# Kernel optimization log

Measured on AMD Instinct MI355X. Metric: run time of the kernel, lower is better.

The kernel has to match this reference:

```python
import jax, jax.numpy as jnp
import numpy as np

HEADS = 16
DHEAD = 128
B, S, DMODEL = 2, 2048, 2048


def setup_inputs() -> dict:
    key = jax.random.key(0)
    k1, k2, k3 = jax.random.split(key, 3)
    x = jax.random.normal(k1, (B, S, DMODEL), dtype=jnp.float32)
    # Linear weights, stored as [in, out] so forward is x @ w (no bias).
    w_in = jax.random.normal(k2, (DMODEL, 3 * HEADS * DHEAD), dtype=jnp.float32) * (DMODEL ** -0.5)
    w_out = jax.random.normal(k3, (HEADS * DHEAD, DMODEL), dtype=jnp.float32) * ((HEADS * DHEAD) ** -0.5)
    # Causal mask: True = masked (strictly upper triangular), broadcast over batch & heads.
    mask = jnp.triu(jnp.ones((S, S), dtype=jnp.bool_), k=1)[None, None, :, :]
    return {"x": x, "w_in": w_in, "w_out": w_out, "mask": mask}


def reference(x, w_in, w_out, mask):
    b, s, _ = x.shape
    # Fused QKV projection: [b,s,3*H*dh] -> [b,s,H,3*dh] -> chunk into q,k,v [b,s,H,dh]
    projected = (x @ w_in).reshape(b, s, HEADS, 3 * DHEAD)
    q, k, v = jnp.split(projected, 3, axis=-1)
    # Scores [b,H,l,L], scaled by 1/sqrt(dhead)
    scale = 1.0 / (DHEAD ** 0.5)
    a = jnp.einsum("blhd,bLhd->bhlL", q, k) * scale
    a = jnp.where(mask, -jnp.inf, a)
    a = jax.nn.softmax(a, axis=-1)
    # Weighted values -> [b,l,H,dh] -> flatten heads -> output projection
    out = jnp.einsum("bhlL,bLhd->blhd", a, v).reshape(b, s, HEADS * DHEAD)
    return out @ w_out
```

## Files before the change

kernel.cpp:

```cpp
#include <hip/hip_runtime.h>

#define HD    16
#define DH    128
#define BB    2
#define SS    2048
#define DM    2048
#define NQKV  6144
#define MTOT  4096

typedef short   bfx8  __attribute__((ext_vector_type(8)));
typedef float   f32x4 __attribute__((ext_vector_type(4)));

__device__ __forceinline__ unsigned short f2bf(float f) {
  union { float f; unsigned int u; } c; c.f = f;
  unsigned int u = c.u + 0x7FFFu + ((c.u >> 16) & 1u);
  return (unsigned short)(u >> 16);
}

__device__ __forceinline__ void gload_lds16(const unsigned short* g, unsigned short* l) {
  __builtin_amdgcn_global_load_lds(
      (const __attribute__((address_space(1))) unsigned int*)g,
      (__attribute__((address_space(3))) unsigned int*)l, 16, 0, 0);
}

#define BARS() do { __builtin_amdgcn_sched_barrier(0); __builtin_amdgcn_s_barrier(); \
                    __builtin_amdgcn_sched_barrier(0); } while (0)
#define VMCNT7() do { asm volatile("s_waitcnt vmcnt(7)" ::: "memory"); \
                      __builtin_amdgcn_sched_barrier(0); } while (0)

__global__ __launch_bounds__(256) void f32_to_bf16_k(const float* __restrict__ in,
                                                     unsigned short* __restrict__ out, int n4) {
  int i = (blockIdx.x * 256 + threadIdx.x);
  if (i >= n4) return;
  const float4 v = *(const float4*)(in + (size_t)i * 4);
  ushort4 o;
  o.x = f2bf(v.x); o.y = f2bf(v.y); o.z = f2bf(v.z); o.w = f2bf(v.w);
  *(ushort4*)(out + (size_t)i * 4) = o;
}

__global__ __launch_bounds__(256) void transpose_f32_bf16_k(const float* __restrict__ in,
                                                            unsigned short* __restrict__ out,
                                                            int R, int C) {
  __shared__ float t[32][33];
  const int c0 = blockIdx.x * 32, r0 = blockIdx.y * 32;
  const int tx = threadIdx.x & 31, ty = threadIdx.x >> 5;
#pragma unroll
  for (int i = 0; i < 4; i++) {
    int r = r0 + ty + i * 8;
    t[ty + i * 8][tx] = in[(size_t)r * C + c0 + tx];
  }
  __syncthreads();
#pragma unroll
  for (int i = 0; i < 4; i++) {
    int c = c0 + ty + i * 8;
    out[(size_t)c * R + r0 + tx] = f2bf(t[tx][ty + i * 8]);
  }
}

__global__ __launch_bounds__(512, 2) void gemm256_qkv_k(const unsigned short* __restrict__ A,
                                                        const unsigned short* __restrict__ Bt,
                                                        unsigned short* __restrict__ Qg,
                                                        unsigned short* __restrict__ Kg,
                                                        unsigned short* __restrict__ Vg,
                                                        int K) {
  __shared__ __align__(16) unsigned short Asb[2][256 * 64];
  __shared__ __align__(16) unsigned short Bsb[2][192 * 64];
  const int tid = threadIdx.x;
  const int lane = tid & 63, wid = tid >> 6;
  const int wr = wid >> 2, wc = wid & 3;
  const int cbase = lane & 15, rgrp = lane >> 4;
  const int bid = (int)blockIdx.x;
  const int id = (bid & 7) * 64 + (bid >> 3);
  const int nb = id >> 4, mb = id & 15;
  const size_t m0 = (size_t)mb * 256, n0 = (size_t)nb * 192;
  const int nkt = K >> 6;

#define STAGE_A64(u_, g_) do {                                                          \
    const int uc_ = ((u_) < nkt ? (u_) : (nkt - 1));                                    \
    const int r_ = tid >> 3, s_ = tid & 7;                                              \
    gload_lds16(A + (m0 + (g_) * 64 + r_) * (size_t)K + uc_ * 64 +                      \
                    (((s_ * 16) ^ ((r_ & 7) << 4)) >> 1),                               \
                &Asb[(u_) & 1][(g_) * 4096] + tid * 8); } while (0)
#define STAGE_B64(u_, g_) do {                                                          \
    const int uc_ = ((u_) < nkt ? (u_) : (nkt - 1));                                    \
    const int r_ = tid >> 3, s_ = tid & 7;                                              \
    gload_lds16(Bt + (n0 + (g_) * 64 + r_) * (size_t)K + uc_ * 64 +                     \
                    (((s_ * 16) ^ ((r_ & 7) << 4)) >> 1),                               \
                &Bsb[(u_) & 1][(g_) * 4096] + tid * 8); } while (0)

  const int axor = (cbase & 7) << 4;
  int a_off[2], b_off[2];
#pragma unroll
  for (int ks = 0; ks < 2; ks++) {
    a_off[ks] = ((wr * 128 + cbase) * 128 + ((ks * 64 + rgrp * 16) ^ axor)) >> 1;
    b_off[ks] = ((wc * 48 + cbase) * 128 + ((ks * 64 + rgrp * 16) ^ axor)) >> 1;
  }

#define RD_A03(dst_, p_) do { _Pragma("unroll")                                          \
    for (int mf_ = 0; mf_ < 4; mf_++) { _Pragma("unroll")                                \
      for (int ks_ = 0; ks_ < 2; ks_++)                                                  \
        dst_[mf_][ks_] = *(const bfx8*)((p_) + a_off[ks_] + mf_ * 1024); } } while (0)
#define RD_A47(dst_, p_) do { _Pragma("unroll")                                          \
    for (int mf_ = 0; mf_ < 4; mf_++) { _Pragma("unroll")                                \
      for (int ks_ = 0; ks_ < 2; ks_++)                                                  \
        dst_[mf_][ks_] = *(const bfx8*)((p_) + a_off[ks_] + (mf_ + 4) * 1024); } } while (0)
#define RD_B01(dst_, p_) do { _Pragma("unroll")                                          \
    for (int nf_ = 0; nf_ < 2; nf_++) { _Pragma("unroll")                                \
      for (int ks_ = 0; ks_ < 2; ks_++)                                                  \
        dst_[nf_][ks_] = *(const bfx8*)((p_) + b_off[ks_] + nf_ * 1024); } } while (0)
#define RD_B2(dst_, p_) do { _Pragma("unroll")                                           \
    for (int ks_ = 0; ks_ < 2; ks_++)                                                    \
      dst_[0][ks_] = *(const bfx8*)((p_) + b_off[ks_] + 2 * 1024); } while (0)

#define MFMA_2N(mo_, AF_, BF_) do {                                                      \
    __builtin_amdgcn_s_setprio(1);                                                      \
    _Pragma("unroll")                                                                    \
    for (int mf_ = 0; mf_ < 4; mf_++) { _Pragma("unroll")                                \
      for (int nf_ = 0; nf_ < 2; nf_++) { _Pragma("unroll")                              \
        for (int ks_ = 0; ks_ < 2; ks_++)                                                \
          acc[mf_ + (mo_)][nf_] = __builtin_amdgcn_mfma_f32_16x16x32_bf16(               \
              AF_[mf_][ks_], BF_[nf_][ks_], acc[mf_ + (mo_)][nf_], 0, 0, 0); } }         \
    __builtin_amdgcn_s_setprio(0); } while (0)

  f32x4 acc[8][3];
  const f32x4 z = {0.f, 0.f, 0.f, 0.f};
#pragma unroll
  for (int mf = 0; mf < 8; mf++)
#pragma unroll
    for (int nf = 0; nf < 3; nf++) acc[mf][nf] = z;

  STAGE_A64(0, 0); STAGE_A64(0, 1); STAGE_A64(0, 2); STAGE_A64(0, 3);
  STAGE_B64(0, 0); STAGE_B64(0, 1); STAGE_B64(0, 2);
  STAGE_A64(1, 0); STAGE_A64(1, 1); STAGE_A64(1, 2); STAGE_A64(1, 3);
  STAGE_B64(1, 0); STAGE_B64(1, 1); STAGE_B64(1, 2);
  VMCNT7();
  BARS();
  bfx8 a03A[4][2], b01A[2][2], a03B[4][2], b01B[2][2];
  RD_A03(a03A, &Asb[0][0]);
  RD_B01(b01A, &Bsb[0][0]);

#define TILE_BODY(u_, A03c, B01c, A03n, B01n) do {                                       \
    const unsigned short* As_  = &Asb[(u_) & 1][0];                                      \
    const unsigned short* Bs_  = &Bsb[(u_) & 1][0];                                      \
    const unsigned short* Asn_ = &Asb[((u_) + 1) & 1][0];                                \
    const unsigned short* Bsn_ = &Bsb[((u_) + 1) & 1][0];                                \
    bfx8 a47[4][2], b2[1][2];                                                            \
               \
    RD_A47(a47, As_);                                                                    \
    STAGE_A64((u_) + 2, 0); STAGE_A64((u_) + 2, 2);                                      \
    BARS();                                                                              \
    MFMA_2N(0, A03c, B01c);                                                              \
                     \
    RD_B2(b2, Bs_);                                                                      \
    STAGE_A64((u_) + 2, 1); STAGE_A64((u_) + 2, 3);                                      \
    BARS();                                                                              \
    MFMA_2N(4, a47, B01c);                                                               \
     \
                                     \
    STAGE_B64((u_) + 2, 0); STAGE_B64((u_) + 2, 1); STAGE_B64((u_) + 2, 2);              \
    VMCNT7();                                                                            \
    BARS();                                                                              \
    RD_A03(A03n, Asn_);                                                                  \
    RD_B01(B01n, Bsn_);                                                                  \
    __builtin_amdgcn_s_setprio(1);                                                      \
    _Pragma("unroll")                                                                    \
    for (int mf_ = 0; mf_ < 4; mf_++) { _Pragma("unroll")                                \
      for (int ks_ = 0; ks_ < 2; ks_++) {                                                \
        acc[mf_][2] = __builtin_amdgcn_mfma_f32_16x16x32_bf16(                           \
            A03c[mf_][ks_], b2[0][ks_], acc[mf_][2], 0, 0, 0);                           \
        acc[mf_ + 4][2] = __builtin_amdgcn_mfma_f32_16x16x32_bf16(                       \
            a47[mf_][ks_], b2[0][ks_], acc[mf_ + 4][2], 0, 0, 0);                        \
      } }                                                                                \
    __builtin_amdgcn_s_setprio(0);                                                      \
    BARS();                                                                              \
  } while (0)

#pragma unroll 1
  for (int u = 0; u < nkt; u += 2) {
    TILE_BODY(u,     a03A, b01A, a03B, b01B);
    TILE_BODY(u + 1, a03B, b01B, a03A, b01A);
  }
#undef TILE_BODY
#undef STAGE_A64
#undef STAGE_B64

#pragma unroll
  for (int mf = 0; mf < 8; mf++)
#pragma unroll
    for (int nf = 0; nf < 3; nf++) {
      const int nn = (int)n0 + wc * 48 + nf * 16;
      const int h = nn / 384, tt = (nn >> 7) % 3;
      const int d = (nn & 127) + cbase;
      const int row0 = (int)m0 + wr * 128 + mf * 16 + rgrp * 4;
      const int bb = row0 >> 11;
      const int s0 = row0 & 2047;
      if (tt == 2) {
        ushort4 v;
        v.x = f2bf(acc[mf][nf][0]); v.y = f2bf(acc[mf][nf][1]);
        v.z = f2bf(acc[mf][nf][2]); v.w = f2bf(acc[mf][nf][3]);
        *(ushort4*)(Vg + ((size_t)(bb * HD + h) * DH + d) * SS + s0) = v;
      } else {
        unsigned short* dst = (tt == 0 ? Qg : Kg);
#pragma unroll
        for (int r = 0; r < 4; r++)
          dst[((size_t)(bb * HD + h) * SS + s0 + r) * DH + d] = f2bf(acc[mf][nf][r]);
      }
    }
}

__global__ __launch_bounds__(256) void gemm_out_k(const unsigned short* __restrict__ A,
                                                  const unsigned short* __restrict__ Bt,
                                                  float* __restrict__ C, int K, int ldc) {
  __shared__ __align__(16) unsigned short As[128 * 32];
  __shared__ __align__(16) unsigned short Bs[128 * 32];
  const int tid = threadIdx.x;
  const int lane = tid & 63, wid = tid >> 6;
  const int wr = wid >> 1, wc = wid & 1;
  const int cbase = lane & 15, rgrp = lane >> 4;
  const size_t m0 = (size_t)blockIdx.y * 128, n0 = (size_t)blockIdx.x * 128;

  f32x4 acc[4][4];
  const f32x4 z = {0.f, 0.f, 0.f, 0.f};
#pragma unroll
  for (int mf = 0; mf < 4; mf++)
#pragma unroll
    for (int nf = 0; nf < 4; nf++) acc[mf][nf] = z;

  const int nkt = K >> 5;
  for (int kt = 0; kt < nkt; ++kt) {
#pragma unroll
    for (int i = 0; i < 2; i++) {
      int idx = i * 256 + tid;
      int row = idx >> 2, cb = idx & 3;
      gload_lds16(A + (m0 + row) * K + (kt * 32 + cb * 8), As + idx * 8);
      gload_lds16(Bt + (n0 + row) * K + (kt * 32 + cb * 8), Bs + idx * 8);
    }
    __syncthreads();
    bfx8 af[4], bfr[4];
#pragma unroll
    for (int mf = 0; mf < 4; mf++)
      af[mf] = *(const bfx8*)(As + (wr * 64 + mf * 16 + cbase) * 32 + rgrp * 8);
#pragma unroll
    for (int nf = 0; nf < 4; nf++)
      bfr[nf] = *(const bfx8*)(Bs + (wc * 64 + nf * 16 + cbase) * 32 + rgrp * 8);
#pragma unroll
    for (int mf = 0; mf < 4; mf++)
#pragma unroll
      for (int nf = 0; nf < 4; nf++)
        acc[mf][nf] = __builtin_amdgcn_mfma_f32_16x16x32_bf16(af[mf], bfr[nf], acc[mf][nf], 0, 0, 0);
    __syncthreads();
  }

#pragma unroll
  for (int mf = 0; mf < 4; mf++)
#pragma unroll
    for (int nf = 0; nf < 4; nf++)
#pragma unroll
      for (int r = 0; r < 4; r++) {
        size_t row = m0 + wr * 64 + mf * 16 + rgrp * 4 + r;
        size_t col = n0 + wc * 64 + nf * 16 + cbase;
        C[row * ldc + col] = acc[mf][nf][r];
      }
}

__global__ __launch_bounds__(256) void attn_fwd_k(const unsigned short* __restrict__ Qg,
                                                  const unsigned short* __restrict__ Kg,
                                                  const unsigned short* __restrict__ Vg,
                                                  unsigned short* __restrict__ ao) {
  __shared__ __align__(16) unsigned short Klds[2][64 * 128];
  __shared__ __align__(16) unsigned short Vt[2][128 * 64];
  __shared__ __align__(16) unsigned short Plds[4][16 * 64];
  const int tid = threadIdx.x;
  const int lane = tid & 63, wid = tid >> 6;
  const int cbase = lane & 15, rgrp = lane >> 4;
  const int cx = (cbase & 7) << 4;

  const int bid = (int)blockIdx.x;
  const int bh = (bid & 7) * 4 + ((bid >> 3) & 3);
  const int qt = 31 - (bid >> 5);
  const int b = bh >> 4, h = bh & 15;
  const int qbase = qt * 64;

  const unsigned short* qp0 = Qg + (size_t)(b * HD + h) * SS * DH;
  const unsigned short* kp  = Kg + (size_t)(b * HD + h) * SS * DH;
  const unsigned short* vp  = Vg + (size_t)(b * HD + h) * DH * SS;
  const float scale = 0.08838834764831845f;
  const f32x4 z = {0.f, 0.f, 0.f, 0.f};
  const int qi = qbase + wid * 16 + cbase;

  bfx8 qf[4];
  {
    const unsigned short* qp = qp0 + (size_t)qi * DH;
#pragma unroll
    for (int ks = 0; ks < 4; ks++) qf[ks] = *(const bfx8*)(qp + ks * 32 + rgrp * 8);
  }

  float m_run = -1e30f, l_run = 0.f;
  f32x4 o[8];
#pragma unroll
  for (int mb = 0; mb < 8; mb++) o[mb] = z;

#define STAGE_T(t_, s_) do {                                                        \
    const int kvb_ = (t_) * 64;                                                     \
    _Pragma("unroll")                                                               \
    for (int i_ = 0; i_ < 4; i_++) {                                                \
      int idx_ = i_ * 256 + tid;                                                    \
      int r_ = idx_ >> 4, bo_ = (idx_ & 15) * 16;                                   \
      gload_lds16(kp + (size_t)(kvb_ + r_) * DH + ((bo_ ^ ((r_ & 7) << 4)) >> 1),   \
                  &Klds[s_][idx_ * 8]);                                             \
    }                                                                               \
    _Pragma("unroll")                                                               \
    for (int i_ = 0; i_ < 4; i_++) {                                                \
      int idx_ = i_ * 256 + tid;                                                    \
      int d_ = idx_ >> 3, bo_ = (idx_ & 7) * 16;                                    \
      gload_lds16(vp + (size_t)d_ * SS + kvb_ + ((bo_ ^ ((d_ & 7) << 4)) >> 1),     \
                  &Vt[s_][idx_ * 8]);                                               \
    } } while (0)

  const int ntiles = qt + 1;
  STAGE_T(0, 0);
  __syncthreads();

  for (int t = 0; t < ntiles; ++t) {
    const int sel = t & 1;
    if (t + 1 < ntiles) STAGE_T(t + 1, sel ^ 1);
    const unsigned short* Ks_ = &Klds[sel][0];
    const unsigned short* Vs_ = &Vt[sel][0];
    const int kvb = t * 64;

    f32x4 s[4];
#pragma unroll
    for (int mf = 0; mf < 4; mf++) s[mf] = z;
#pragma unroll
    for (int mf = 0; mf < 4; mf++)
#pragma unroll
      for (int ks = 0; ks < 4; ks++) {
        bfx8 kf = *(const bfx8*)(Ks_ + (((mf * 16 + cbase) * 256 + ((ks * 64 + rgrp * 16) ^ cx)) >> 1));
        s[mf] = __builtin_amdgcn_mfma_f32_16x16x32_bf16(kf, qf[ks], s[mf], 0, 0, 0);
      }

    float sv[4][4];
    const bool diag = (t == ntiles - 1);
#pragma unroll
    for (int mf = 0; mf < 4; mf++)
#pragma unroll
      for (int r = 0; r < 4; r++) {
        float v = s[mf][r] * scale;
        if (diag && (kvb + mf * 16 + rgrp * 4 + r > qi)) v = -1e30f;
        sv[mf][r] = v;
      }
    float tm = sv[0][0];
#pragma unroll
    for (int mf = 0; mf < 4; mf++)
#pragma unroll
      for (int r = 0; r < 4; r++) tm = fmaxf(tm, sv[mf][r]);
    tm = fmaxf(tm, __shfl_xor(tm, 16));
    tm = fmaxf(tm, __shfl_xor(tm, 32));
    const float mnew = fmaxf(m_run, tm);
    float p[4][4];
    float rs = 0.f;
#pragma unroll
    for (int mf = 0; mf < 4; mf++)
#pragma unroll
      for (int r = 0; r < 4; r++) { p[mf][r] = __expf(sv[mf][r] - mnew); rs += p[mf][r]; }
    rs += __shfl_xor(rs, 16);
    rs += __shfl_xor(rs, 32);
    const float alpha = __expf(m_run - mnew);
    l_run = l_run * alpha + rs;
    m_run = mnew;
#pragma unroll
    for (int mb = 0; mb < 8; mb++)
#pragma unroll
      for (int r = 0; r < 4; r++) o[mb][r] *= alpha;

#pragma unroll
    for (int mf = 0; mf < 4; mf++)
#pragma unroll
      for (int rr = 0; rr < 2; rr++) {
        unsigned int pp = (unsigned int)f2bf(p[mf][2 * rr]) |
                          ((unsigned int)f2bf(p[mf][2 * rr + 1]) << 16);
        *(unsigned int*)((char*)&Plds[wid][0] +
                         (cbase * 128 + ((mf * 32 + rgrp * 8 + rr * 4) ^ cx))) = pp;
      }
    bfx8 pf[2];
#pragma unroll
    for (int k2 = 0; k2 < 2; k2++)
      pf[k2] = *(const bfx8*)((const char*)&Plds[wid][0] +
                              (cbase * 128 + ((k2 * 64 + rgrp * 16) ^ cx)));

#pragma unroll
    for (int mb = 0; mb < 8; mb++)
#pragma unroll
      for (int k2 = 0; k2 < 2; k2++) {
        bfx8 vf = *(const bfx8*)(Vs_ + (((mb * 16 + cbase) * 128 + ((k2 * 64 + rgrp * 16) ^ cx)) >> 1));
        o[mb] = __builtin_amdgcn_mfma_f32_16x16x32_bf16(vf, pf[k2], o[mb], 0, 0, 0);
      }
    __syncthreads();
  }
#undef STAGE_T

  const float rinv = 1.0f / l_run;
  unsigned short* aop = ao + ((size_t)(b * SS + qi)) * DM + h * DH + rgrp * 4;
#pragma unroll
  for (int mb = 0; mb < 8; mb++) {
    ushort4 v;
    v.x = f2bf(o[mb][0] * rinv); v.y = f2bf(o[mb][1] * rinv);
    v.z = f2bf(o[mb][2] * rinv); v.w = f2bf(o[mb][3] * rinv);
    *(ushort4*)(aop + mb * 16) = v;
  }
}

extern "C" void kernel_launch(void* const* d_in, const int* in_sizes, int n_in,
                              void* d_out, int out_size, void* d_ws, size_t ws_size,
                              hipStream_t stream) {
  (void)in_sizes; (void)n_in; (void)out_size; (void)ws_size;
  const float* x     = (const float*)d_in[0];
  const float* w_in  = (const float*)d_in[1];
  const float* w_out = (const float*)d_in[2];
  float* out = (float*)d_out;

  char* ws = (char*)d_ws;
  unsigned short* Xb  = (unsigned short*)(ws);
  unsigned short* Wit = (unsigned short*)(ws + (16ull << 20));
  unsigned short* Wot = (unsigned short*)(ws + (40ull << 20));
  unsigned short* Qg  = (unsigned short*)(ws + (48ull << 20));
  unsigned short* Kg  = (unsigned short*)(ws + (64ull << 20));
  unsigned short* Vg  = (unsigned short*)(ws + (80ull << 20));
  unsigned short* AO  = (unsigned short*)(ws + (96ull << 20));

  f32_to_bf16_k<<<MTOT * DM / 4 / 256, 256, 0, stream>>>(x, Xb, MTOT * DM / 4);
  transpose_f32_bf16_k<<<dim3(NQKV / 32, DM / 32), 256, 0, stream>>>(w_in, Wit, DM, NQKV);
  transpose_f32_bf16_k<<<dim3(DM / 32, DM / 32), 256, 0, stream>>>(w_out, Wot, DM, DM);
  gemm256_qkv_k<<<512, 512, 0, stream>>>(Xb, Wit, Qg, Kg, Vg, DM);
  attn_fwd_k<<<1024, 256, 0, stream>>>(Qg, Kg, Vg, AO);
  gemm_out_k<<<dim3(DM / 128, MTOT / 128), 256, 0, stream>>>(AO, Wot, out, DM, DM);
}
```

Before: 253.8 us.

## Replace output GEMM with 256x128 double-buffered swizzled pipelined kernel

Swaps the simple 128x128 output-projection GEMM, which synchronises twice per K step, for a 256x128 tile kernel with 512 threads. It reuses the QKV GEMM's pipeline: double-buffered LDS filled by global_load_lds, an XOR swizzle against bank conflicts, and loads issued two tiles ahead with vmcnt waits. It also remaps block ids for L2 locality. The aim is to overlap memory with MFMA and cut the sync and LDS stall overhead, at the cost of more LDS per block and fewer blocks (256).

```diff
diff --git a/kernel.cpp b/kernel.cpp
--- a/kernel.cpp
+++ b/kernel.cpp
@@ -26,6 +26,8 @@
 #define BARS() do { __builtin_amdgcn_sched_barrier(0); __builtin_amdgcn_s_barrier(); \
                     __builtin_amdgcn_sched_barrier(0); } while (0)
 #define VMCNT7() do { asm volatile("s_waitcnt vmcnt(7)" ::: "memory"); \
+                      __builtin_amdgcn_sched_barrier(0); } while (0)
+#define VMCNT6() do { asm volatile("s_waitcnt vmcnt(6)" ::: "memory"); \
                       __builtin_amdgcn_sched_barrier(0); } while (0)
 
 __global__ __launch_bounds__(256) void f32_to_bf16_k(const float* __restrict__ in,
@@ -145,18 +147,14 @@
     const unsigned short* Asn_ = &Asb[((u_) + 1) & 1][0];                                \
     const unsigned short* Bsn_ = &Bsb[((u_) + 1) & 1][0];                                \
     bfx8 a47[4][2], b2[1][2];                                                            \
-               \
     RD_A47(a47, As_);                                                                    \
     STAGE_A64((u_) + 2, 0); STAGE_A64((u_) + 2, 2);                                      \
     BARS();                                                                              \
     MFMA_2N(0, A03c, B01c);                                                              \
-                     \
     RD_B2(b2, Bs_);                                                                      \
     STAGE_A64((u_) + 2, 1); STAGE_A64((u_) + 2, 3);                                      \
     BARS();                                                                              \
     MFMA_2N(4, a47, B01c);                                                               \
-     \
-                                     \
     STAGE_B64((u_) + 2, 0); STAGE_B64((u_) + 2, 1); STAGE_B64((u_) + 2, 2);              \
     VMCNT7();                                                                            \
     BARS();                                                                              \
@@ -208,57 +206,109 @@
     }
 }
 
-__global__ __launch_bounds__(256) void gemm_out_k(const unsigned short* __restrict__ A,
-                                                  const unsigned short* __restrict__ Bt,
-                                                  float* __restrict__ C, int K, int ldc) {
-  __shared__ __align__(16) unsigned short As[128 * 32];
-  __shared__ __align__(16) unsigned short Bs[128 * 32];
+__global__ __launch_bounds__(512, 2) void gemm256_out_k(const unsigned short* __restrict__ A,
+                                                        const unsigned short* __restrict__ Bt,
+                                                        float* __restrict__ C, int K, int ldc) {
+  __shared__ __align__(16) unsigned short Asb[2][256 * 64];
+  __shared__ __align__(16) unsigned short Bsb[2][128 * 64];
   const int tid = threadIdx.x;
   const int lane = tid & 63, wid = tid >> 6;
-  const int wr = wid >> 1, wc = wid & 1;
+  const int wr = wid >> 2, wc = wid & 3;
   const int cbase = lane & 15, rgrp = lane >> 4;
-  const size_t m0 = (size_t)blockIdx.y * 128, n0 = (size_t)blockIdx.x * 128;
-
-  f32x4 acc[4][4];
+  const int bid = (int)blockIdx.x;
+  const int id = (bid & 7) * 32 + (bid >> 3);
+  const int nb = id >> 4, mb = id & 15;
+  const size_t m0 = (size_t)mb * 256, n0 = (size_t)nb * 128;
+  const int nkt = K >> 6;
+
+#define STAGE_AO(u_, g_) do {                                                           \
+    const int uc_ = ((u_) < nkt ? (u_) : (nkt - 1));                                    \
+    const int r_ = tid >> 3, s_ = tid & 7;                                              \
+    gload_lds16(A + (m0 + (g_) * 64 + r_) * (size_t)K + uc_ * 64 +                      \
+                    (((s_ * 16) ^ ((r_ & 7) << 4)) >> 1),                               \
+                &Asb[(u_) & 1][(g_) * 4096] + tid * 8); } while (0)
+#define STAGE_BO(u_, g_) do {                                                           \
+    const int uc_ = ((u_) < nkt ? (u_) : (nkt - 1));                                    \
+    const int r_ = tid >> 3, s_ = tid & 7;                                              \
+    gload_lds16(Bt + (n0 + (g_) * 64 + r_) * (size_t)K + uc_ * 64 +                     \
+                    (((s_ * 16) ^ ((r_ & 7) << 4)) >> 1),                               \
+                &Bsb[(u_) & 1][(g_) * 4096] + tid * 8); } while (0)
+
+  const int axor = (cbase & 7) << 4;
+  int a_off[2], b_off[2];
+#pragma unroll
+  for (int ks = 0; ks < 2; ks++) {
+    a_off[ks] = ((wr * 128 + cbase) * 128 + ((ks * 64 + rgrp * 16) ^ axor)) >> 1;
+    b_off[ks] = ((wc * 32 + cbase) * 128 + ((ks * 64 + rgrp * 16) ^ axor)) >> 1;
+  }
+
+#define MFMA_O(mo_, AF_, BF_) do {                                                       \
+    __builtin_amdgcn_s_setprio(1);                                                      \
+    _Pragma("unroll")                                                                    \
+    for (int mf_ = 0; mf_ < 4; mf_++) { _Pragma("unroll")                                \
+      for (int nf_ = 0; nf_ < 2; nf_++) { _Pragma("unroll")                              \
+        for (int ks_ = 0; ks_ < 2; ks_++)                                                \
+          acc[mf_ + (mo_)][nf_] = __builtin_amdgcn_mfma_f32_16x16x32_bf16(               \
+              AF_[mf_][ks_], BF_[nf_][ks_], acc[mf_ + (mo_)][nf_], 0, 0, 0); } }         \
+    __builtin_amdgcn_s_setprio(0); } while (0)
+
+  f32x4 acc[8][2];
   const f32x4 z = {0.f, 0.f, 0.f, 0.f};
 #pragma unroll
-  for (int mf = 0; mf < 4; mf++)
-#pragma unroll
-    for (int nf = 0; nf < 4; nf++) acc[mf][nf] = z;
-
-  const int nkt = K >> 5;
-  for (int kt = 0; kt < nkt; ++kt) {
-#pragma unroll
-    for (int i = 0; i < 2; i++) {
-      int idx = i * 256 + tid;
-      int row = idx >> 2, cb = idx & 3;
-      gload_lds16(A + (m0 + row) * K + (kt * 32 + cb * 8), As + idx * 8);
-      gload_lds16(Bt + (n0 + row) * K + (kt * 32 + cb * 8), Bs + idx * 8);
-    }
-    __syncthreads();
-    bfx8 af[4], bfr[4];
-#pragma unroll
-    for (int mf = 0; mf < 4; mf++)
-      af[mf] = *(const bfx8*)(As + (wr * 64 + mf * 16 + cbase) * 32 + rgrp * 8);
-#pragma unroll
-    for (int nf = 0; nf < 4; nf++)
-      bfr[nf] = *(const bfx8*)(Bs + (wc * 64 + nf * 16 + cbase) * 32 + rgrp * 8);
-#pragma unroll
-    for (int mf = 0; mf < 4; mf++)
-#pragma unroll
-      for (int nf = 0; nf < 4; nf++)
-        acc[mf][nf] = __builtin_amdgcn_mfma_f32_16x16x32_bf16(af[mf], bfr[nf], acc[mf][nf], 0, 0, 0);
-    __syncthreads();
-  }
-
-#pragma unroll
-  for (int mf = 0; mf < 4; mf++)
-#pragma unroll
-    for (int nf = 0; nf < 4; nf++)
+  for (int mf = 0; mf < 8; mf++)
+#pragma unroll
+    for (int nf = 0; nf < 2; nf++) acc[mf][nf] = z;
+
+  STAGE_AO(0, 0); STAGE_AO(0, 1); STAGE_AO(0, 2); STAGE_AO(0, 3);
+  STAGE_BO(0, 0); STAGE_BO(0, 1);
+  STAGE_AO(1, 0); STAGE_AO(1, 1); STAGE_AO(1, 2); STAGE_AO(1, 3);
+  STAGE_BO(1, 0); STAGE_BO(1, 1);
+  VMCNT6();
+  BARS();
+  bfx8 a03A[4][2], b01A[2][2], a03B[4][2], b01B[2][2];
+  RD_A03(a03A, &Asb[0][0]);
+  RD_B01(b01A, &Bsb[0][0]);
+
+#define TILE_BODY_O(u_, A03c, B01c, A03n, B01n) do {                                     \
+    const unsigned short* As_  = &Asb[(u_) & 1][0];                                      \
+    const unsigned short* Bs_  = &Bsb[(u_) & 1][0];                                      \
+    const unsigned short* Asn_ = &Asb[((u_) + 1) & 1][0];                                \
+    const unsigned short* Bsn_ = &Bsb[((u_) + 1) & 1][0];                                \
+    bfx8 a47[4][2];                                                                      \
+    \
+    RD_A47(a47, As_);                                                                    \
+    STAGE_AO((u_) + 2, 0); STAGE_AO((u_) + 2, 2);                                        \
+    BARS();                                                                              \
+    MFMA_O(0, A03c, B01c);                                                               \
+     \
+               \
+    STAGE_AO((u_) + 2, 1); STAGE_AO((u_) + 2, 3);                                        \
+    STAGE_BO((u_) + 2, 0); STAGE_BO((u_) + 2, 1);                                        \
+    VMCNT6();                                                                            \
+    BARS();                                                                              \
+    RD_A03(A03n, Asn_);                                                                  \
+    RD_B01(B01n, Bsn_);                                                                  \
+    MFMA_O(4, a47, B01c);                                                                \
+    BARS();                                                                              \
+  } while (0)
+
+#pragma unroll 1
+  for (int u = 0; u < nkt; u += 2) {
+    TILE_BODY_O(u,     a03A, b01A, a03B, b01B);
+    TILE_BODY_O(u + 1, a03B, b01B, a03A, b01A);
+  }
+#undef TILE_BODY_O
+#undef STAGE_AO
+#undef STAGE_BO
+
+#pragma unroll
+  for (int mf = 0; mf < 8; mf++)
+#pragma unroll
+    for (int nf = 0; nf < 2; nf++)
 #pragma unroll
       for (int r = 0; r < 4; r++) {
-        size_t row = m0 + wr * 64 + mf * 16 + rgrp * 4 + r;
-        size_t col = n0 + wc * 64 + nf * 16 + cbase;
+        size_t row = m0 + wr * 128 + mf * 16 + rgrp * 4 + r;
+        size_t col = n0 + wc * 32 + nf * 16 + cbase;
         C[row * ldc + col] = acc[mf][nf][r];
       }
 }
@@ -433,5 +483,5 @@
   transpose_f32_bf16_k<<<dim3(DM / 32, DM / 32), 256, 0, stream>>>(w_out, Wot, DM, DM);
   gemm256_qkv_k<<<512, 512, 0, stream>>>(Xb, Wit, Qg, Kg, Vg, DM);
   attn_fwd_k<<<1024, 256, 0, stream>>>(Qg, Kg, Vg, AO);
-  gemm_out_k<<<dim3(DM / 128, MTOT / 128), 256, 0, stream>>>(AO, Wot, out, DM, DM);
-}
+  gemm256_out_k<<<256, 512, 0, stream>>>(AO, Wot, out, DM, DM);
+}
```

Measured after the change: 235.2 us. 7.3% less time.
